# Optimization experiments

Measured on AMD Instinct MI355X. Metric: run time of the kernel, lower is better.

The kernel has to match this reference:

```python
import jax, jax.numpy as jnp
import numpy as np
import math

# ---- static configuration (mirrors FluidPCConfig defaults) ----
B, S, D = 8, 2048, 2048
N_LEVELS = 3
OUTER = 3            # fluid_outer_iters
HORIZON = 4          # mpc_horizon
INNER_STEPS = 5      # mpc_inner_steps
INNER_LR = 0.1       # mpc_inner_lr
CFL = 0.4            # cfl_target
KAPPA0 = 0.01        # kappa_init
LERAY_ITERS = 50     # leray_max_iter (fixed trip count; see notes)
REACT_STEPS = 1
REACT_ETA = 0.1
R2 = 1.4142135623730951


def _normalize(rho, eps=1e-8):
    rho = jnp.abs(rho) + eps
    return rho / jnp.sum(rho, axis=-1, keepdims=True)


def haar_dwt(x, n_levels):
    """Packed 1D Haar DWT along the sequence axis. x: (B,S,D) -> (B,S,D)."""
    a = x
    dets = []
    for _ in range(n_levels):
        e, o = a[:, 0::2], a[:, 1::2]
        dets.append((e - o) / R2)
        a = (e + o) / R2
    # layout: [approx_L, detail_L, detail_{L-1}, ..., detail_1]
    return jnp.concatenate([a] + dets[::-1], axis=1)


def haar_idwt(c, n_levels):
    """Inverse of haar_dwt. c: (B,S,D) -> (B,S,D)."""
    S_ = c.shape[1]
    a = c[:, : S_ >> n_levels]
    off = S_ >> n_levels
    for lev in range(n_levels, 0, -1):
        L = S_ >> lev
        d = c[:, off:off + L]
        off += L
        e, o = (a + d) / R2, (a - d) / R2
        a = jnp.stack([e, o], axis=2).reshape(c.shape[0], 2 * L, c.shape[2])
    return a


def coeffs_to_rho(c):
    # per-node scalar density from D-dim coefficients: (B,S,D) -> (B,S)
    return jnp.sqrt(jnp.sum(c * c, axis=-1))


# ---- periodic 1D graph operators on the S wavelet-coefficient nodes ----
def grad1(p):
    return jnp.roll(p, -1, axis=-1) - p


def div1(u):
    return u - jnp.roll(u, 1, axis=-1)


def lap1(p):
    return jnp.roll(p, -1, axis=-1) + jnp.roll(p, 1, axis=-1) - 2.0 * p


def leray(u):
    """Leray projection: u <- u - grad(p), lap(p)=div(u), Jacobi sweeps."""
    b = div1(u)
    def body(i, p):
        return 0.5 * (jnp.roll(p, -1, axis=-1) + jnp.roll(p, 1, axis=-1) - b)
    p = jax.lax.fori_loop(0, LERAY_ITERS, body, jnp.zeros_like(u))
    return u - grad1(p)


def rescale_dt(u):
    # per-batch dt so that achieved CFL == cfl_target: (B,S) -> (B,)
    return CFL / (jnp.max(jnp.abs(u), axis=-1) + 1e-8)


def advect(rho, u, dt, kappa):
    """Conservative upwind advection + kappa-weighted diffusion."""
    dt = dt[:, None]
    F = jnp.where(u > 0, u * rho, u * jnp.roll(rho, -1, axis=-1))
    return rho - dt * (F - jnp.roll(F, 1, axis=-1)) + kappa * dt * lap1(rho)


def mpc(rho, v):
    """Inner-gradient MPC drift (non-differentiable branch: stop_gradient)."""
    rho = jax.lax.stop_gradient(rho)
    v = jax.lax.stop_gradient(v)

    def cost(u):
        r = rho
        for _ in range(HORIZON):
            up = leray(u)
            r = _normalize(advect(r, up, rescale_dt(up), 0.0))
        # expected distance to value field
        return jnp.mean(jnp.sum((1.0 - v) * r, axis=-1))

    u = grad1(v)  # init drift toward high-value nodes
    g = jax.grad(cost)
    for _ in range(INNER_STEPS):
        u = u - INNER_LR * g(u)
    return u


def reaction(rho, phi):
    """Predictive-coding reaction: mirror-descent on potential+entropy."""
    for _ in range(REACT_STEPS):
        g = phi[None, :] + jnp.log(rho)
        rho = _normalize(rho * jnp.exp(-REACT_ETA * g))
    return rho


def kappa_at(k):
    # cosine anneal from KAPPA0 at k=0 to 0 at k=OUTER-1
    return 0.5 * KAPPA0 * (1.0 + math.cos(math.pi * k / (OUTER - 1)))


# static band index: node -> wavelet band (0=approx, 1..N_LEVELS=details)
_bi = np.zeros(S, dtype=np.int32)
_off = S >> N_LEVELS
for _i, _lev in enumerate(range(N_LEVELS, 0, -1)):
    _L = S >> _lev
    _bi[_off:_off + _L] = _i + 1
    _off += _L
BAND_IDX = jnp.asarray(_bi)


def setup_inputs() -> dict:
    key = jax.random.key(0)
    k1, k2, k3, k4 = jax.random.split(key, 4)
    return {
        "x": jax.random.normal(k1, (B, S, D), dtype=jnp.float32),
        "w_val": jax.random.normal(k2, (D,), dtype=jnp.float32) / np.float32(np.sqrt(D)),
        "phi": jax.random.normal(k3, (S,), dtype=jnp.float32) * 0.1,
        "band_w": jax.random.normal(k4, (N_LEVELS + 1, D), dtype=jnp.float32),
    }


def reference(x, w_val, phi, band_w):
    # density field from wavelet coefficients of x
    rho = _normalize(coeffs_to_rho(haar_dwt(x, N_LEVELS)))
    # value field: Linear(D,1) head, broadcast over D, DWT-packed, normalized
    per_token = jnp.einsum("bsd,d->bs", x, w_val)
    v_sig = jnp.broadcast_to(per_token[:, :, None], (B, S, D))
    v = _normalize(coeffs_to_rho(haar_dwt(v_sig, N_LEVELS)))

    for k in range(OUTER):
        rho = reaction(rho, phi)
        u = leray(mpc(rho, v))
        dt = rescale_dt(u)
        rho = _normalize(advect(rho, u, dt, kappa_at(k)))

    rho_f = rho + 0.1 * v
    rho_f = rho_f / jnp.sum(rho_f, axis=-1, keepdims=True)
    # readout: per-band learned D-vector, then inverse DWT -> (B,S,D)
    coeffs = rho_f[:, :, None] * band_w[BAND_IDX]
    return haar_idwt(coeffs, N_LEVELS)
```

## Files before the change

### kernel.cpp

```cpp
#include <hip/hip_runtime.h>
#include <math.h>

#define NSEQ 2048
#define EPSF 1e-8f
#define INV2R2 0.35355339059327373f
#define INVR2  0.7071067811865476f
#define NT 512

struct Taps65 { float v[65]; };

constexpr Taps65 make_taps65() {
  Taps65 t{};
  double K[99] = {};
  for (int j = -49; j <= 49; ++j) {
    int aj = j < 0 ? -j : j;
    double term = 1.0;
    for (int q = 0; q < aj; ++q) term *= 0.5;
    double sum = term;
    for (int i = aj + 2; i <= 49; i += 2) {
      int m = (i + j) / 2;
      term *= (double)((i - 1) * i) / (4.0 * (double)m * (double)(i - m));
      sum += term;
    }
    K[j + 49] = -0.5 * sum;
  }
  for (int o = -32; o <= 32; ++o) {
    double km1 = K[o - 1 + 49], k0 = K[o + 49], kp1 = K[o + 1 + 49];
    double T = kp1 - 2.0 * k0 + km1;
    t.v[o + 32] = (float)(((o == 0) ? 1.0 : 0.0) - T);
  }
  return t;
}
constexpr Taps65 LK65 = make_taps65();

__device__ __forceinline__ float wave_sum(float x) {
#pragma unroll
  for (int m = 1; m < 64; m <<= 1) x += __shfl_xor(x, m, 64);
  return x;
}
__device__ __forceinline__ float wave_max(float x) {
#pragma unroll
  for (int m = 1; m < 64; m <<= 1) x = fmaxf(x, __shfl_xor(x, m, 64));
  return x;
}
__device__ __forceinline__ float block_sum(float x, float* red, int tid, int& gen) {
  float w = wave_sum(x);
  int slot = (gen & 7) << 5; gen++;
  if ((tid & 63) == 0) red[slot + (tid >> 6)] = w;
  __syncthreads();
  float4 a = *(float4*)(red + slot), b = *(float4*)(red + slot + 4);
  return ((a.x + a.y) + (a.z + a.w)) + ((b.x + b.y) + (b.z + b.w));
}
__device__ __forceinline__ void block_sum2(float a, float b, float* red, int tid, int& gen,
                                           float& oa, float& ob) {
  float wa = wave_sum(a), wb = wave_sum(b);
  int slot = (gen & 7) << 5; gen++;
  if ((tid & 63) == 0) { int w = tid >> 6; red[slot + w] = wa; red[slot + 16 + w] = wb; }
  __syncthreads();
  float4 a0 = *(float4*)(red + slot),      a1 = *(float4*)(red + slot + 4);
  float4 b0 = *(float4*)(red + slot + 16), b1 = *(float4*)(red + slot + 20);
  oa = ((a0.x + a0.y) + (a0.z + a0.w)) + ((a1.x + a1.y) + (a1.z + a1.w));
  ob = ((b0.x + b0.y) + (b0.z + b0.w)) + ((b1.x + b1.y) + (b1.z + b1.w));
}
__device__ __forceinline__ float sgnf(float x) {
  return (x > 0.f) ? 1.f : ((x < 0.f) ? -1.f : 0.f);
}

__device__ __forceinline__ void conv65(const float in[4], float acc[4],
                                       float* __restrict__ cbuf, int tid) {
  *(float4*)(cbuf + (tid << 2)) = make_float4(in[0], in[1], in[2], in[3]);
  __syncthreads();
  const int base = tid << 2;
  acc[0] = 0.f; acc[1] = 0.f; acc[2] = 0.f; acc[3] = 0.f;
#pragma unroll
  for (int m = 0; m < 17; ++m) {
    const int idx = (base - 32 + 4 * m) & (NSEQ - 1);
    const float4 c4 = *(const float4*)(cbuf + idx);
    const float cv[4] = {c4.x, c4.y, c4.z, c4.w};
#pragma unroll
    for (int jj = 0; jj < 4; ++jj) {
      const int d = 4 * m + jj;
#pragma unroll
      for (int j = 0; j < 4; ++j) {
        const int o = d - 32 - j;
        if (o >= -32 && o <= 32) acc[j] = fmaf(LK65.v[o + 32], cv[jj], acc[j]);
      }
    }
  }
}

__global__ __launch_bounds__(256) void kA(const float* __restrict__ x,
                                          const float* __restrict__ wv,
                                          float* __restrict__ rho_us,
                                          float* __restrict__ pt) {
  const int blk = blockIdx.x;
  const int b = blk >> 8;
  const int g = blk & 255;
  const float* xb = x + (((size_t)b * NSEQ) + (size_t)g * 8) * 2048;
  const int tid = threadIdx.x;
  float sq[8] = {0.f, 0.f, 0.f, 0.f, 0.f, 0.f, 0.f, 0.f};
  float pp[8] = {0.f, 0.f, 0.f, 0.f, 0.f, 0.f, 0.f, 0.f};
  for (int c = tid * 4; c < 2048; c += 1024) {
    float4 w4 = *(const float4*)(wv + c);
    float wj[4] = {w4.x, w4.y, w4.z, w4.w};
    float xv[8][4];
#pragma unroll
    for (int r = 0; r < 8; ++r) {
      float4 t = *(const float4*)(xb + (size_t)r * 2048 + c);
      xv[r][0] = t.x; xv[r][1] = t.y; xv[r][2] = t.z; xv[r][3] = t.w;
    }
#pragma unroll
    for (int j = 0; j < 4; ++j) {
      float x0 = xv[0][j], x1 = xv[1][j], x2 = xv[2][j], x3 = xv[3][j];
      float x4 = xv[4][j], x5 = xv[5][j], x6 = xv[6][j], x7 = xv[7][j];
      float t01 = x0 + x1, t23 = x2 + x3, t45 = x4 + x5, t67 = x6 + x7;
      float a = t01 + t23, bb = t45 + t67;
      float c3 = a + bb, d3 = a - bb, d2a = t01 - t23, d2b = t45 - t67;
      float d10 = x0 - x1, d11 = x2 - x3, d12 = x4 - x5, d13 = x6 - x7;
      sq[0] += c3 * c3;  sq[1] += d3 * d3;  sq[2] += d2a * d2a; sq[3] += d2b * d2b;
      sq[4] += d10 * d10; sq[5] += d11 * d11; sq[6] += d12 * d12; sq[7] += d13 * d13;
      float w = wj[j];
      pp[0] += x0 * w; pp[1] += x1 * w; pp[2] += x2 * w; pp[3] += x3 * w;
      pp[4] += x4 * w; pp[5] += x5 * w; pp[6] += x6 * w; pp[7] += x7 * w;
    }
  }
  __shared__ float sred[4][16];
  float vals[16];
#pragma unroll
  for (int q = 0; q < 8; ++q) vals[q] = sq[q];
#pragma unroll
  for (int q = 0; q < 8; ++q) vals[8 + q] = pp[q];
#pragma unroll
  for (int q = 0; q < 16; ++q) vals[q] = wave_sum(vals[q]);
  int lane = tid & 63, wid = tid >> 6;
  if (lane == 0) {
#pragma unroll
    for (int q = 0; q < 16; ++q) sred[wid][q] = vals[q];
  }
  __syncthreads();
  if (tid < 16) {
    float s = sred[0][tid] + sred[1][tid] + sred[2][tid] + sred[3][tid];
    if (tid < 8) {
      float scale = (tid < 2) ? 0.125f : ((tid < 4) ? 0.25f : 0.5f);
      int pos = (tid == 0) ? g : (tid == 1) ? (256 + g)
               : (tid < 4) ? (512 + 2 * g + (tid - 2)) : (1024 + 4 * g + (tid - 4));
      rho_us[b * NSEQ + pos] = sqrtf(s * scale);
    } else {
      pt[b * NSEQ + 8 * g + (tid - 8)] = s;
    }
  }
}

__global__ __launch_bounds__(NT, 2) void kB(const float* __restrict__ rho_us,
                                            const float* __restrict__ pt,
                                            const float* __restrict__ phi,
                                            float* __restrict__ rho_f) {
  __shared__ float cb[2][NSEQ];
  __shared__ float vE0[NT];
  __shared__ float rhoE0[NT], rhoE3[NT];
  __shared__ float upE3[NT];
  __shared__ float yE0[3][NT], yE3[3][NT];
  __shared__ float4 pairE[2][NT];
  __shared__ float red[256];
  __shared__ float red2[8];

  const int tid = threadIdx.x;
  const int b = blockIdx.x;
  const int tm1 = (tid - 1) & (NT - 1);
  const int tp1 = (tid + 1) & (NT - 1);
  int gen = 0, cc = 0;
  const float CFL_ = 0.4f;

  float4 phv = *(const float4*)(phi + 4 * tid);
  float phir[4] = {phv.x, phv.y, phv.z, phv.w};

  float v_r[4]; float vp4c;
  {
    const float* ptb = pt + b * NSEQ;
    float vl[4]; float part = 0.f;
#pragma unroll
    for (int j = 0; j < 4; ++j) {
      float c;
      if (tid < 64) {
        int r = (4 * tid + j) * 8;
        float t01 = ptb[r] + ptb[r+1], t23 = ptb[r+2] + ptb[r+3];
        float t45 = ptb[r+4] + ptb[r+5], t67 = ptb[r+6] + ptb[r+7];
        c = ((t01 + t23) + (t45 + t67)) * INV2R2;
      } else if (tid < 128) {
        int r = (4 * (tid - 64) + j) * 8;
        float t01 = ptb[r] + ptb[r+1], t23 = ptb[r+2] + ptb[r+3];
        float t45 = ptb[r+4] + ptb[r+5], t67 = ptb[r+6] + ptb[r+7];
        c = ((t01 + t23) - (t45 + t67)) * INV2R2;
      } else if (tid < 256) {
        int r = (4 * (tid - 128) + j) * 4;
        c = ((ptb[r] + ptb[r+1]) - (ptb[r+2] + ptb[r+3])) * 0.5f;
      } else {
        int r = (4 * (tid - 256) + j) * 2;
        c = (ptb[r] - ptb[r+1]) * INVR2;
      }
      float val = sqrtf(2048.0f * c * c) + EPSF;
      vl[j] = val; part += val;
    }
    float sv = block_sum(part, red, tid, gen);
    float inv = 1.0f / sv;
#pragma unroll
    for (int j = 0; j < 4; ++j) v_r[j] = vl[j] * inv;
    vE0[tid] = v_r[0];
  }
  float rho_r[4];
  {
    float4 rv = *(const float4*)(rho_us + b * NSEQ + 4 * tid);
    float rl[4] = {rv.x + EPSF, rv.y + EPSF, rv.z + EPSF, rv.w + EPSF};
    float part = rl[0] + rl[1] + rl[2] + rl[3];
    float sr = block_sum(part, red, tid, gen);
    float inv = 1.f / sr;
#pragma unroll
    for (int j = 0; j < 4; ++j) rho_r[j] = rl[j] * inv;
  }
  vp4c = vE0[tp1];

  for (int k = 0; k < 3; ++k) {
    {
      float tl[4]; float part = 0.f;
#pragma unroll
      for (int j = 0; j < 4; ++j) {
        float r = rho_r[j];
        float t = r * expf(-0.1f * (phir[j] + logf(r)));
        float t2 = fabsf(t) + EPSF;
        tl[j] = t2; part += t2;
      }
      float s = block_sum(part, red, tid, gen);
      float inv = 1.f / s;
#pragma unroll
      for (int j = 0; j < 4; ++j) rho_r[j] = tl[j] * inv;
      rhoE0[tid] = rho_r[0]; rhoE3[tid] = rho_r[3];
    }
    float u_r[4];
    u_r[0] = v_r[1] - v_r[0]; u_r[1] = v_r[2] - v_r[1];
    u_r[2] = v_r[3] - v_r[2]; u_r[3] = vp4c - v_r[3];

    float up_r[4], y_r[4][4], ym1c[3], yp4c2[3];
    for (int step = 0; step < 5; ++step) {
      conv65(u_r, up_r, cb[(cc++) & 1], tid);
      upE3[tid] = up_r[3];
      {
        float mm = fmaxf(fmaxf(fabsf(up_r[0]), fabsf(up_r[1])),
                         fmaxf(fabsf(up_r[2]), fabsf(up_r[3])));
        mm = wave_max(mm);
        if ((tid & 63) == 0) red2[tid >> 6] = mm;
      }
      __syncthreads();
      float4 r2a = *(float4*)(red2), r2b = *(float4*)(red2 + 4);
      float mx = fmaxf(fmaxf(fmaxf(r2a.x, r2a.y), fmaxf(r2a.z, r2a.w)),
                       fmaxf(fmaxf(r2b.x, r2b.y), fmaxf(r2b.z, r2b.w)));
      float um1 = upE3[tm1];
      float rhom1 = rhoE3[tm1], rhop4 = rhoE0[tp1];
      float dt = CFL_ / (mx + EPSF);
      float sarr[4]; float spv = 1.f; float ntie = 1.f, dot = 0.f;
#pragma unroll
      for (int h = 0; h < 4; ++h) {
        float invp = 1.f / spv;
        if (h >= 1) { ym1c[h-1] = yE3[h-1][tm1]; yp4c2[h-1] = yE0[h-1][tp1]; }
        float rr[6];
        if (h == 0) {
          rr[0] = rhom1; rr[1] = rho_r[0]; rr[2] = rho_r[1];
          rr[3] = rho_r[2]; rr[4] = rho_r[3]; rr[5] = rhop4;
        } else {
          rr[0] = (fabsf(ym1c[h-1]) + EPSF) * invp;
#pragma unroll
          for (int j = 0; j < 4; ++j) rr[j+1] = (fabsf(y_r[h-1][j]) + EPSF) * invp;
          rr[5] = (fabsf(yp4c2[h-1]) + EPSF) * invp;
        }
        float part2 = 0.f, aux = 0.f;
#pragma unroll
        for (int j = 0; j < 4; ++j) {
          float ri = rr[j+1], rim1 = rr[j], rip1 = rr[j+2];
          float ui = up_r[j], um = j ? up_r[j-1] : um1;
          float Fi = ui > 0.f ? ui * ri : ui * rip1;
          float Fm = um > 0.f ? um * rim1 : um * ri;
          float yv = ri - dt * (Fi - Fm);
          y_r[h][j] = yv;
          float ayv = fabsf(yv) + EPSF;
          part2 += ayv;
          if (h == 0) aux += (fabsf(ui) == mx) ? 1.f : 0.f;
          if (h == 3) aux += (1.f - v_r[j]) * 0.125f * ayv;
        }
        if (h < 3) { yE0[h][tid] = y_r[h][0]; yE3[h][tid] = y_r[h][3]; }
        if (h == 3) {
          float sg0 = sgnf(y_r[3][0]), sg3 = sgnf(y_r[3][3]);
          pairE[1][tid] = make_float4(sg0 * (1.f - v_r[0]) * 0.125f, sg0,
                                      sg3 * (1.f - v_r[3]) * 0.125f, sg3);
        }
        if (h == 0) { float o1, o2; block_sum2(part2, aux, red, tid, gen, o1, o2); sarr[0] = o1; ntie = o2; }
        else if (h == 3) { float o1, o2; block_sum2(part2, aux, red, tid, gen, o1, o2); sarr[3] = o1; dot = o2 / o1; }
        else sarr[h] = block_sum(part2, red, tid, gen);
        spv = sarr[h];
      }
      float wreg[4], upbar[4];
#pragma unroll
      for (int j = 0; j < 4; ++j) { wreg[j] = (1.f - v_r[j]) * 0.125f; upbar[j] = 0.f; }
      float dtb_part = 0.f;
#pragma unroll
      for (int h = 3; h >= 0; --h) {
        float invst = 1.f / sarr[h];
        float invp = (h > 0) ? 1.f / sarr[h-1] : 0.f;
        const int bo = h & 1;
        float yb_r[4];
#pragma unroll
        for (int j = 0; j < 4; ++j)
          yb_r[j] = sgnf(y_r[h][j]) * (wreg[j] - dot) * invst;
        float4 pm = pairE[bo][tm1], pp = pairE[bo][tp1];
        float ybm1 = (pm.z - dot * pm.w) * invst;
        float ybp4 = (pp.x - dot * pp.y) * invst;
        float rr[6];
        if (h == 0) {
          rr[0] = rhom1; rr[1] = rho_r[0]; rr[2] = rho_r[1];
          rr[3] = rho_r[2]; rr[4] = rho_r[3]; rr[5] = rhop4;
        } else {
          rr[0] = (fabsf(ym1c[h-1]) + EPSF) * invp;
#pragma unroll
          for (int j = 0; j < 4; ++j) rr[j+1] = (fabsf(y_r[h-1][j]) + EPSF) * invp;
          rr[5] = (fabsf(yp4c2[h-1]) + EPSF) * invp;
        }
        float dotn = 0.f;
#pragma unroll
        for (int j = 0; j < 4; ++j) {
          float ri = rr[j+1], rim1 = rr[j], rip1 = rr[j+2];
          float ui = up_r[j], um = j ? up_r[j-1] : um1;
          float ybi = yb_r[j];
          float ybm = j ? yb_r[j-1] : ybm1;
          float ybp = (j < 3) ? yb_r[j+1] : ybp4;
          float Fbi = dt * (ybp - ybi);
          float Fbm = dt * (ybi - ybm);
          float wn = ybi;
          if (ui > 0.f)    wn += Fbi * ui;
          if (!(um > 0.f)) wn += Fbm * um;
          upbar[j] += Fbi * (ui > 0.f ? ri : rip1);
          float Fi = ui > 0.f ? ui * ri : ui * rip1;
          float Fm = um > 0.f ? um * rim1 : um * ri;
          dtb_part -= ybi * (Fi - Fm);
          if (h > 0) dotn += wn * ri;
          wreg[j] = wn;
        }
        if (h > 0) {
          float sgA = sgnf(y_r[h-1][0]), sgB = sgnf(y_r[h-1][3]);
          pairE[(h - 1) & 1][tid] = make_float4(sgA * wreg[0], sgA, sgB * wreg[3], sgB);
          dot = block_sum(dotn, red, tid, gen);
        }
      }
      float dtbar = block_sum(dtb_part, red, tid, gen);
      float md = mx + EPSF;
      float mbar = dtbar * (-CFL_ / (md * md));
      float tiesc = mbar / ntie;
#pragma unroll
      for (int j = 0; j < 4; ++j) {
        float ui = up_r[j];
        if (fabsf(ui) == mx) upbar[j] += tiesc * sgnf(ui);
      }
      float accv[4];
      conv65(upbar, accv, cb[(cc++) & 1], tid);
#pragma unroll
      for (int j = 0; j < 4; ++j) u_r[j] -= 0.1f * accv[j];
    }
    conv65(u_r, up_r, cb[(cc++) & 1], tid);
    upE3[tid] = up_r[3];
    {
      float mm = fmaxf(fmaxf(fabsf(up_r[0]), fabsf(up_r[1])),
                       fmaxf(fabsf(up_r[2]), fabsf(up_r[3])));
      mm = wave_max(mm);
      if ((tid & 63) == 0) red2[tid >> 6] = mm;
    }
    __syncthreads();
    float4 r2a = *(float4*)(red2), r2b = *(float4*)(red2 + 4);
    float mx = fmaxf(fmaxf(fmaxf(r2a.x, r2a.y), fmaxf(r2a.z, r2a.w)),
                     fmaxf(fmaxf(r2b.x, r2b.y), fmaxf(r2b.z, r2b.w)));
    float um1 = upE3[tm1];
    float rhom1 = rhoE3[tm1], rhop4 = rhoE0[tp1];
    float dt = CFL_ / (mx + EPSF);
    float kap = (k == 0) ? 0.01f : ((k == 1) ? 0.005f : 0.0f);
    float rr[6];
    rr[0] = rhom1; rr[1] = rho_r[0]; rr[2] = rho_r[1];
    rr[3] = rho_r[2]; rr[4] = rho_r[3]; rr[5] = rhop4;
    float ylc[4]; float p2 = 0.f;
#pragma unroll
    for (int j = 0; j < 4; ++j) {
      float ri = rr[j+1], rim1 = rr[j], rip1 = rr[j+2];
      float ui = up_r[j], um = j ? up_r[j-1] : um1;
      float Fi = ui > 0.f ? ui * ri : ui * rip1;
      float Fm = um > 0.f ? um * rim1 : um * ri;
      float yv = ri - dt * (Fi - Fm) + kap * dt * (rip1 + rim1 - 2.f * ri);
      ylc[j] = yv; p2 += fabsf(yv) + EPSF;
    }
    float s = block_sum(p2, red, tid, gen);
    float inv = 1.f / s;
#pragma unroll
    for (int j = 0; j < 4; ++j) rho_r[j] = (fabsf(ylc[j]) + EPSF) * inv;
    rhoE0[tid] = rho_r[0]; rhoE3[tid] = rho_r[3];
  }
  {
    float fl[4]; float part = 0.f;
#pragma unroll
    for (int j = 0; j < 4; ++j) {
      float f = rho_r[j] + 0.1f * v_r[j];
      fl[j] = f; part += f;
    }
    float s = block_sum(part, red, tid, gen);
    float inv = 1.f / s;
    *(float4*)(rho_f + b * NSEQ + 4 * tid) =
        make_float4(fl[0] * inv, fl[1] * inv, fl[2] * inv, fl[3] * inv);
  }
}

__global__ __launch_bounds__(256) void kC(const float* __restrict__ rho_f,
                                          const float* __restrict__ bw,
                                          float* __restrict__ out) {
  const int blk = blockIdx.x;
  const int b = blk >> 8;
  const int g = blk & 255;
  __shared__ float q[8];
  if (threadIdx.x < 8) {
    int t = threadIdx.x;
    const float* rb = rho_f + b * NSEQ;
    float val;
    if (t == 0)      val = rb[g] * INV2R2;
    else if (t == 1) val = rb[256 + g] * INV2R2;
    else if (t < 4)  val = rb[512 + 2 * g + (t - 2)] * 0.5f;
    else             val = rb[1024 + 4 * g + (t - 4)] * INVR2;
    q[t] = val;
  }
  __syncthreads();
  float* ob = out + (((size_t)b * NSEQ) + (size_t)g * 8) * 2048;
  for (int c = threadIdx.x * 4; c < 2048; c += 1024) {
    float4 B0 = *(const float4*)(bw + c);
    float4 B1 = *(const float4*)(bw + 2048 + c);
    float4 B2 = *(const float4*)(bw + 4096 + c);
    float4 B3 = *(const float4*)(bw + 6144 + c);
    float b0[4] = {B0.x, B0.y, B0.z, B0.w};
    float b1[4] = {B1.x, B1.y, B1.z, B1.w};
    float b2[4] = {B2.x, B2.y, B2.z, B2.w};
    float b3[4] = {B3.x, B3.y, B3.z, B3.w};
    float o[8][4];
#pragma unroll
    for (int cc = 0; cc < 4; ++cc) {
      float pa = q[0] * b0[cc], pd3 = q[1] * b1[cc];
      float p2a = q[2] * b2[cc], p2b = q[3] * b2[cc];
      float e0 = pa + pd3, e1 = pa - pd3;
      float f0 = e0 + p2a, f1 = e0 - p2a, f2 = e1 + p2b, f3 = e1 - p2b;
      float g0 = q[4] * b3[cc], g1 = q[5] * b3[cc], g2 = q[6] * b3[cc], g3 = q[7] * b3[cc];
      o[0][cc] = f0 + g0; o[1][cc] = f0 - g0;
      o[2][cc] = f1 + g1; o[3][cc] = f1 - g1;
      o[4][cc] = f2 + g2; o[5][cc] = f2 - g2;
      o[6][cc] = f3 + g3; o[7][cc] = f3 - g3;
    }
#pragma unroll
    for (int j = 0; j < 8; ++j) {
      float4 t = make_float4(o[j][0], o[j][1], o[j][2], o[j][3]);
      *(float4*)(ob + (size_t)j * 2048 + c) = t;
    }
  }
}

extern "C" void kernel_launch(void* const* d_in, const int* in_sizes, int n_in,
                              void* d_out, int out_size, void* d_ws, size_t ws_size,
                              hipStream_t stream) {
  (void)in_sizes; (void)n_in; (void)out_size; (void)ws_size;
  const float* x   = (const float*)d_in[0];
  const float* wv  = (const float*)d_in[1];
  const float* phi = (const float*)d_in[2];
  const float* bw  = (const float*)d_in[3];
  float* out = (float*)d_out;
  float* rho_us = (float*)d_ws;
  float* pt     = rho_us + 8 * NSEQ;
  float* rho_f  = pt + 8 * NSEQ;

  kA<<<dim3(2048), dim3(256), 0, stream>>>(x, wv, rho_us, pt);
  kB<<<dim3(8), dim3(NT), 0, stream>>>(rho_us, pt, phi, rho_f);
  kC<<<dim3(2048), dim3(256), 0, stream>>>(rho_f, bw, out);
}
```

Measured before the change: 181.3 us.

## Fold preconditioner convolutions into squared kernel and hoist invariant initial projection

Precomputes the composed 129-tap kernel LK*LK so the per-step gradient update is applied directly to the projected velocity, eliminating one 65-tap convolution and its barrier per inner step. The initial projected velocity and its max are computed once and reused across outer iterations. This cuts barriers and redundant work, at the cost of a wider stencil and slightly different rounding from the composed truncated taps.

```diff
diff --git a/kernel.cpp b/kernel.cpp
--- a/kernel.cpp
+++ b/kernel.cpp
@@ -7,10 +7,10 @@
 #define INVR2  0.7071067811865476f
 #define NT 512
 
-struct Taps65 { float v[65]; };
-
-constexpr Taps65 make_taps65() {
-  Taps65 t{};
+struct TapsAll { float lk65[65]; float lk2[129]; };
+
+constexpr TapsAll make_taps() {
+  TapsAll t{};
   double K[99] = {};
   for (int j = -49; j <= 49; ++j) {
     int aj = j < 0 ? -j : j;
@@ -24,14 +24,24 @@
     }
     K[j + 49] = -0.5 * sum;
   }
-  for (int o = -32; o <= 32; ++o) {
-    double km1 = K[o - 1 + 49], k0 = K[o + 49], kp1 = K[o + 1 + 49];
-    double T = kp1 - 2.0 * k0 + km1;
-    t.v[o + 32] = (float)(((o == 0) ? 1.0 : 0.0) - T);
+  double LKd[101] = {};
+  for (int o = -50; o <= 50; ++o) {
+    double km1 = (o - 1 >= -49 && o - 1 <= 49) ? K[o - 1 + 49] : 0.0;
+    double k0  = (o     >= -49 && o     <= 49) ? K[o + 49]     : 0.0;
+    double kp1 = (o + 1 >= -49 && o + 1 <= 49) ? K[o + 1 + 49] : 0.0;
+    LKd[o + 50] = ((o == 0) ? 1.0 : 0.0) - (kp1 - 2.0 * k0 + km1);
+  }
+  for (int o = -32; o <= 32; ++o) t.lk65[o + 32] = (float)LKd[o + 50];
+  for (int o = -64; o <= 64; ++o) {
+    double s = 0.0;
+    int alo = (o - 50 > -50) ? o - 50 : -50;
+    int ahi = (o + 50 <  50) ? o + 50 :  50;
+    for (int a = alo; a <= ahi; ++a) s += LKd[a + 50] * LKd[o - a + 50];
+    t.lk2[o + 64] = (float)s;
   }
   return t;
 }
-constexpr Taps65 LK65 = make_taps65();
+constexpr TapsAll TAPS = make_taps();
 
 __device__ __forceinline__ float wave_sum(float x) {
 #pragma unroll
@@ -67,15 +77,15 @@
 }
 
 __device__ __forceinline__ void conv65(const float in[4], float acc[4],
-                                       float* __restrict__ cbuf, int tid) {
-  *(float4*)(cbuf + (tid << 2)) = make_float4(in[0], in[1], in[2], in[3]);
+                                       float* __restrict__ cb, int tid) {
+  *(float4*)(cb + (tid << 2)) = make_float4(in[0], in[1], in[2], in[3]);
   __syncthreads();
   const int base = tid << 2;
   acc[0] = 0.f; acc[1] = 0.f; acc[2] = 0.f; acc[3] = 0.f;
 #pragma unroll
   for (int m = 0; m < 17; ++m) {
     const int idx = (base - 32 + 4 * m) & (NSEQ - 1);
-    const float4 c4 = *(const float4*)(cbuf + idx);
+    const float4 c4 = *(const float4*)(cb + idx);
     const float cv[4] = {c4.x, c4.y, c4.z, c4.w};
 #pragma unroll
     for (int jj = 0; jj < 4; ++jj) {
@@ -83,7 +93,30 @@
 #pragma unroll
       for (int j = 0; j < 4; ++j) {
         const int o = d - 32 - j;
-        if (o >= -32 && o <= 32) acc[j] = fmaf(LK65.v[o + 32], cv[jj], acc[j]);
+        if (o >= -32 && o <= 32) acc[j] = fmaf(TAPS.lk65[o + 32], cv[jj], acc[j]);
+      }
+    }
+  }
+}
+
+__device__ __forceinline__ void conv129(const float in[4], float acc[4],
+                                        float* __restrict__ cb, int tid) {
+  *(float4*)(cb + (tid << 2)) = make_float4(in[0], in[1], in[2], in[3]);
+  __syncthreads();
+  const int base = tid << 2;
+  acc[0] = 0.f; acc[1] = 0.f; acc[2] = 0.f; acc[3] = 0.f;
+#pragma unroll
+  for (int m = 0; m < 33; ++m) {
+    const int idx = (base - 64 + 4 * m) & (NSEQ - 1);
+    const float4 c4 = *(const float4*)(cb + idx);
+    const float cv[4] = {c4.x, c4.y, c4.z, c4.w};
+#pragma unroll
+    for (int jj = 0; jj < 4; ++jj) {
+      const int d = 4 * m + jj;
+#pragma unroll
+      for (int j = 0; j < 4; ++j) {
+        const int o = d - 64 - j;
+        if (o >= -64 && o <= 64) acc[j] = fmaf(TAPS.lk2[o + 64], cv[jj], acc[j]);
       }
     }
   }
@@ -155,7 +188,7 @@
                                             const float* __restrict__ pt,
                                             const float* __restrict__ phi,
                                             float* __restrict__ rho_f) {
-  __shared__ float cb[2][NSEQ];
+  __shared__ float cb[NSEQ];
   __shared__ float vE0[NT];
   __shared__ float rhoE0[NT], rhoE3[NT];
   __shared__ float upE3[NT];
@@ -168,7 +201,7 @@
   const int b = blockIdx.x;
   const int tm1 = (tid - 1) & (NT - 1);
   const int tp1 = (tid + 1) & (NT - 1);
-  int gen = 0, cc = 0;
+  int gen = 0;
   const float CFL_ = 0.4f;
 
   float4 phv = *(const float4*)(phi + 4 * tid);
@@ -219,6 +252,26 @@
   }
   vp4c = vE0[tp1];
 
+  float up_r[4], up0_r[4];
+  float mx, mx0, um1c, um10;
+  {
+    float u0[4] = {v_r[1] - v_r[0], v_r[2] - v_r[1], v_r[3] - v_r[2], vp4c - v_r[3]};
+    conv65(u0, up_r, cb, tid);
+    upE3[tid] = up_r[3];
+    float mm = fmaxf(fmaxf(fabsf(up_r[0]), fabsf(up_r[1])),
+                     fmaxf(fabsf(up_r[2]), fabsf(up_r[3])));
+    mm = wave_max(mm);
+    if ((tid & 63) == 0) red2[tid >> 6] = mm;
+    __syncthreads();
+    float4 r2a = *(float4*)(red2), r2b = *(float4*)(red2 + 4);
+    mx = fmaxf(fmaxf(fmaxf(r2a.x, r2a.y), fmaxf(r2a.z, r2a.w)),
+               fmaxf(fmaxf(r2b.x, r2b.y), fmaxf(r2b.z, r2b.w)));
+    um1c = upE3[tm1];
+#pragma unroll
+    for (int j = 0; j < 4; ++j) up0_r[j] = up_r[j];
+    mx0 = mx; um10 = um1c;
+  }
+
   for (int k = 0; k < 3; ++k) {
     {
       float tl[4]; float part = 0.f;
@@ -235,26 +288,16 @@
       for (int j = 0; j < 4; ++j) rho_r[j] = tl[j] * inv;
       rhoE0[tid] = rho_r[0]; rhoE3[tid] = rho_r[3];
     }
-    float u_r[4];
-    u_r[0] = v_r[1] - v_r[0]; u_r[1] = v_r[2] - v_r[1];
-    u_r[2] = v_r[3] - v_r[2]; u_r[3] = vp4c - v_r[3];
-
-    float up_r[4], y_r[4][4], ym1c[3], yp4c2[3];
+    __syncthreads();
+    const float rhom1 = rhoE3[tm1], rhop4 = rhoE0[tp1];
+    if (k > 0) {
+#pragma unroll
+      for (int j = 0; j < 4; ++j) up_r[j] = up0_r[j];
+      mx = mx0; um1c = um10;
+    }
+
+    float y_r[4][4], ym1c[3], yp4c2[3];
     for (int step = 0; step < 5; ++step) {
-      conv65(u_r, up_r, cb[(cc++) & 1], tid);
-      upE3[tid] = up_r[3];
-      {
-        float mm = fmaxf(fmaxf(fabsf(up_r[0]), fabsf(up_r[1])),
-                         fmaxf(fabsf(up_r[2]), fabsf(up_r[3])));
-        mm = wave_max(mm);
-        if ((tid & 63) == 0) red2[tid >> 6] = mm;
-      }
-      __syncthreads();
-      float4 r2a = *(float4*)(red2), r2b = *(float4*)(red2 + 4);
-      float mx = fmaxf(fmaxf(fmaxf(r2a.x, r2a.y), fmaxf(r2a.z, r2a.w)),
-                       fmaxf(fmaxf(r2b.x, r2b.y), fmaxf(r2b.z, r2b.w)));
-      float um1 = upE3[tm1];
-      float rhom1 = rhoE3[tm1], rhop4 = rhoE0[tp1];
       float dt = CFL_ / (mx + EPSF);
       float sarr[4]; float spv = 1.f; float ntie = 1.f, dot = 0.f;
 #pragma unroll
@@ -275,7 +318,7 @@
 #pragma unroll
         for (int j = 0; j < 4; ++j) {
           float ri = rr[j+1], rim1 = rr[j], rip1 = rr[j+2];
-          float ui = up_r[j], um = j ? up_r[j-1] : um1;
+          float ui = up_r[j], um = j ? up_r[j-1] : um1c;
           float Fi = ui > 0.f ? ui * ri : ui * rip1;
           float Fm = um > 0.f ? um * rim1 : um * ri;
           float yv = ri - dt * (Fi - Fm);
@@ -326,7 +369,7 @@
 #pragma unroll
         for (int j = 0; j < 4; ++j) {
           float ri = rr[j+1], rim1 = rr[j], rip1 = rr[j+2];
-          float ui = up_r[j], um = j ? up_r[j-1] : um1;
+          float ui = up_r[j], um = j ? up_r[j-1] : um1c;
           float ybi = yb_r[j];
           float ybm = j ? yb_r[j-1] : ybm1;
           float ybp = (j < 3) ? yb_r[j+1] : ybp4;
@@ -358,24 +401,22 @@
         if (fabsf(ui) == mx) upbar[j] += tiesc * sgnf(ui);
       }
       float accv[4];
-      conv65(upbar, accv, cb[(cc++) & 1], tid);
-#pragma unroll
-      for (int j = 0; j < 4; ++j) u_r[j] -= 0.1f * accv[j];
-    }
-    conv65(u_r, up_r, cb[(cc++) & 1], tid);
-    upE3[tid] = up_r[3];
-    {
-      float mm = fmaxf(fmaxf(fabsf(up_r[0]), fabsf(up_r[1])),
-                       fmaxf(fabsf(up_r[2]), fabsf(up_r[3])));
-      mm = wave_max(mm);
-      if ((tid & 63) == 0) red2[tid >> 6] = mm;
-    }
-    __syncthreads();
-    float4 r2a = *(float4*)(red2), r2b = *(float4*)(red2 + 4);
-    float mx = fmaxf(fmaxf(fmaxf(r2a.x, r2a.y), fmaxf(r2a.z, r2a.w)),
-                     fmaxf(fmaxf(r2b.x, r2b.y), fmaxf(r2b.z, r2b.w)));
-    float um1 = upE3[tm1];
-    float rhom1 = rhoE3[tm1], rhop4 = rhoE0[tp1];
+      conv129(upbar, accv, cb, tid);
+#pragma unroll
+      for (int j = 0; j < 4; ++j) up_r[j] -= 0.1f * accv[j];
+      upE3[tid] = up_r[3];
+      {
+        float mm = fmaxf(fmaxf(fabsf(up_r[0]), fabsf(up_r[1])),
+                         fmaxf(fabsf(up_r[2]), fabsf(up_r[3])));
+        mm = wave_max(mm);
+        if ((tid & 63) == 0) red2[tid >> 6] = mm;
+      }
+      __syncthreads();
+      float4 r2a = *(float4*)(red2), r2b = *(float4*)(red2 + 4);
+      mx = fmaxf(fmaxf(fmaxf(r2a.x, r2a.y), fmaxf(r2a.z, r2a.w)),
+                 fmaxf(fmaxf(r2b.x, r2b.y), fmaxf(r2b.z, r2b.w)));
+      um1c = upE3[tm1];
+    }
     float dt = CFL_ / (mx + EPSF);
     float kap = (k == 0) ? 0.01f : ((k == 1) ? 0.005f : 0.0f);
     float rr[6];
@@ -385,7 +426,7 @@
 #pragma unroll
     for (int j = 0; j < 4; ++j) {
       float ri = rr[j+1], rim1 = rr[j], rip1 = rr[j+2];
-      float ui = up_r[j], um = j ? up_r[j-1] : um1;
+      float ui = up_r[j], um = j ? up_r[j-1] : um1c;
       float Fi = ui > 0.f ? ui * ri : ui * rip1;
       float Fm = um > 0.f ? um * rim1 : um * ri;
       float yv = ri - dt * (Fi - Fm) + kap * dt * (rip1 + rim1 - 2.f * ri);
@@ -395,7 +436,6 @@
     float inv = 1.f / s;
 #pragma unroll
     for (int j = 0; j < 4; ++j) rho_r[j] = (fabsf(ylc[j]) + EPSF) * inv;
-    rhoE0[tid] = rho_r[0]; rhoE3[tid] = rho_r[3];
   }
   {
     float fl[4]; float part = 0.f;
```

Result: slower. 196.5 us (+8.4%).
